# Optimization experiments

Measured on AMD Instinct MI355X. Metric: run time of the kernel, lower is better.

Reference implementation:

```python
import jax, jax.numpy as jnp
import numpy as np

EPS = 1e-8
SCALE_FACTOR = 5.0
ITERS = 3

def _ln(x, g, b):
    m = x.mean(-1, keepdims=True)
    v = ((x - m) ** 2).mean(-1, keepdims=True)
    return (x - m) / jnp.sqrt(v + 1e-5) * g + b

def setup_inputs() -> dict:
    key = jax.random.key(0)
    ks = jax.random.split(key, 12)
    B, N, K, D = 8, 1024, 8, 256
    n01 = lambda k, s, sc=0.02: jax.random.normal(k, s, jnp.float32) * sc
    return {
        "inputs": jax.random.normal(ks[0], (B, N, D), jnp.float32),
        "conditioning": jax.random.normal(ks[1], (B, K, D + 4), jnp.float32),
        "ni_g": jnp.ones((D,), jnp.float32), "ni_b": jnp.zeros((D,), jnp.float32),
        "ns_g": jnp.ones((D,), jnp.float32), "ns_b": jnp.zeros((D,), jnp.float32),
        "wq": n01(ks[2], (D, D)), "wk": n01(ks[3], (D, D)), "wv": n01(ks[4], (D, D)),
        "gp_w": n01(ks[5], (2, D), 0.5), "gp_b": jnp.zeros((D,), jnp.float32),
        "ge_ln_g": jnp.ones((D,), jnp.float32), "ge_ln_b": jnp.zeros((D,), jnp.float32),
        "ge_w1": n01(ks[6], (D, 2 * D)), "ge_b1": jnp.zeros((2 * D,), jnp.float32),
        "ge_w2": n01(ks[7], (2 * D, D)), "ge_b2": jnp.zeros((D,), jnp.float32),
        "gru_wih": n01(ks[8], (3 * D, D)), "gru_whh": n01(ks[9], (3 * D, D)),
        "gru_bih": jnp.zeros((3 * D,), jnp.float32), "gru_bhh": jnp.zeros((3 * D,), jnp.float32),
    }

def _forward(inputs, conditioning, ni_g, ni_b, ns_g, ns_b, wq, wk, wv,
             gp_w, gp_b, ge_ln_g, ge_ln_b, ge_w1, ge_b1, ge_w2, ge_b2,
             gru_wih, gru_whh, gru_bih, gru_bhh):
    B, N, FD = inputs.shape
    D = wq.shape[1]
    attn_scale = D ** -0.5
    side = int(round(N ** 0.5))
    xs = jnp.linspace(-1.0, 1.0, side)
    abs_grid = jnp.stack(jnp.meshgrid(xs, xs, indexing="ij"), -1).reshape(N, 2)  # (N,2)

    x = _ln(inputs, ni_g, ni_b)
    k = x @ wk  # (B,N,D)
    v = x @ wv  # (B,N,D)

    def grid_enc(t):
        h = _ln(t, ge_ln_g, ge_ln_b)
        h = jax.nn.relu(h @ ge_w1 + ge_b1)
        return h @ ge_w2 + ge_b2

    def step(slots_full, update):
        slots = slots_full[..., :-4]                       # (B,K,D)
        pos = jnp.clip(slots_full[..., -4:-2], -1.0, 1.0)  # (B,K,2)
        scl = jnp.clip(slots_full[..., -2:], 1e-3, 2.0)    # (B,K,2)
        rel_grid = (abs_grid[None, None] - pos[:, :, None]) / (scl[:, :, None] * SCALE_FACTOR)  # (B,K,N,2)
        rel_enc = rel_grid @ gp_w + gp_b                   # (B,K,N,D)
        rel_k = grid_enc(k[:, None] + rel_enc)             # (B,K,N,D)
        rel_v = grid_enc(v[:, None] + rel_enc)             # (B,K,N,D)
        q = _ln(slots, ns_g, ns_b) @ wq                    # (B,K,D)
        dots = jnp.einsum("bkd,bknd->bkn", q, rel_k) * attn_scale
        attn0 = jax.nn.softmax(dots, axis=1)               # softmax over the SLOT axis
        attn = attn0 + EPS
        attn = attn / attn.sum(-1, keepdims=True)
        pos_n = jnp.einsum("bkn,nd->bkd", attn0, abs_grid)
        spread = (abs_grid[None, None] - pos_n[:, :, None]) ** 2  # (B,K,N,2)
        scl_n = jnp.clip(jnp.sqrt(jnp.einsum("bkn,bknd->bkd", attn0 + EPS, spread)), 1e-3, 2.0)
        if update:
            upd = jnp.einsum("bknd,bkn->bkd", rel_v, attn)
            gx = upd @ gru_wih.T + gru_bih
            gh = slots @ gru_whh.T + gru_bhh
            xr, xz, xn = jnp.split(gx, 3, -1)
            hr, hz, hn = jnp.split(gh, 3, -1)
            r = jax.nn.sigmoid(xr + hr)
            z = jax.nn.sigmoid(xz + hz)
            n_ = jnp.tanh(xn + r * hn)
            slots = (1.0 - z) * n_ + z * slots
        return jnp.concatenate([slots, pos_n, scl_n], -1), attn0, rel_grid

    attn0 = rel_grid = None
    for i in range(ITERS + 1):
        conditioning, attn0, rel_grid = step(conditioning, i < ITERS)
    return conditioning, attn0, rel_grid

def reference(inputs, conditioning, ni_g, ni_b, ns_g, ns_b, wq, wk, wv,
              gp_w, gp_b, ge_ln_g, ge_ln_b, ge_w1, ge_b1, ge_w2, ge_b2,
              gru_wih, gru_whh, gru_bih, gru_bhh):
    return _forward(inputs, conditioning, ni_g, ni_b, ns_g, ns_b, wq, wk, wv,
                    gp_w, gp_b, ge_ln_g, ge_ln_b, ge_w1, ge_b1, ge_w2, ge_b2,
                    gru_wih, gru_whh, gru_bih, gru_bhh)
```

## Files before the change

### kernel.cpp

```cpp
#include <hip/hip_runtime.h>
#include <math.h>

#define NB 8
#define NN 1024
#define NK 8
#define ND 256
#define ND2 512
#define NBK 64
#define EPSA 1e-8f
#define LNEPS 1e-5f
#define GSTEP (2.0f/31.0f)

using short8 = __attribute__((ext_vector_type(8))) short;
using short4v = __attribute__((ext_vector_type(4))) short;
using floatx4 = __attribute__((ext_vector_type(4))) float;

__device__ __forceinline__ short f2bf(float f) {
  unsigned u = __builtin_bit_cast(unsigned, f);
  u += 0x7fffu + ((u >> 16) & 1u);
  return (short)(u >> 16);
}
__device__ __forceinline__ float bf2f(short s) {
  unsigned u = ((unsigned)(unsigned short)s) << 16;
  return __builtin_bit_cast(float, u);
}

__global__ __launch_bounds__(256) void k_cvt_all(
    const float* __restrict__ w1, const float* __restrict__ w2,
    const float* __restrict__ wk, const float* __restrict__ wv,
    const float* __restrict__ wih, const float* __restrict__ whh,
    const float* __restrict__ wq, const float* __restrict__ b2,
    const float* __restrict__ gpw, const float* __restrict__ lng,
    const float* __restrict__ lnb, const float* __restrict__ b1,
    short* __restrict__ w1T, short* __restrict__ wkT, short* __restrict__ wvT,
    short* __restrict__ whhp, short* __restrict__ w2B,
    float* __restrict__ bx, float* __restrict__ vb, float* __restrict__ vecs) {
  __shared__ float redS[4][32];
  const int blk = blockIdx.x;
  const int t = threadIdx.x;
  if (blk < 576) {
    const int id4 = blk * 256 + t;
    if (id4 < 32768) {
      const int i = id4 * 4;
      const int k = i >> 9, n0 = i & 511;
      const float4 v = *(const float4*)(w1 + (size_t)k * 512 + n0);
      const float vv[4] = {v.x, v.y, v.z, v.w};
#pragma unroll
      for (int q = 0; q < 4; q++) {
        const int n = n0 + q;
        const int dst = ((n >> 4) * 8 + (k >> 5)) * 512 + ((k >> 3) & 3) * 128 + (n & 15) * 8 + (k & 7);
        w1T[dst] = f2bf(vv[q]);
      }
    } else if (id4 < 49152) {
      const int i = (id4 - 32768) * 4;
      const int k = i >> 8, n0 = i & 255;
      const float4 v = *(const float4*)(wk + (size_t)k * 256 + n0);
      const float vv[4] = {v.x, v.y, v.z, v.w};
#pragma unroll
      for (int q = 0; q < 4; q++) {
        const int n = n0 + q;
        const int dst = ((n >> 4) * 8 + (k >> 5)) * 512 + ((k >> 3) & 3) * 128 + (n & 15) * 8 + (k & 7);
        wkT[dst] = f2bf(vv[q]);
      }
    } else if (id4 < 65536) {
      const int i = (id4 - 49152) * 4;
      const int k = i >> 8, n0 = i & 255;
      const float4 v = *(const float4*)(wv + (size_t)k * 256 + n0);
      const float vv[4] = {v.x, v.y, v.z, v.w};
#pragma unroll
      for (int q = 0; q < 4; q++) {
        const int n = n0 + q;
        const int dst = ((n >> 4) * 8 + (k >> 5)) * 512 + ((k >> 3) & 3) * 128 + (n & 15) * 8 + (k & 7);
        wvT[dst] = f2bf(vv[q]);
      }
    } else if (id4 < 114688) {
      const int i = (id4 - 65536) * 4;
      const int j = i >> 8, d0 = i & 255;
      const float4 v = *(const float4*)(whh + i);
      short4v pk = {f2bf(v.x), f2bf(v.y), f2bf(v.z), f2bf(v.w)};
      *(short4v*)&whhp[(size_t)((d0 >> 3) * 768 + j) * 8 + (d0 & 7)] = pk;
    } else {
      const int i = (id4 - 114688) * 4;
      const float4 v = *(const float4*)(w2 + i);
      short4v pk = {f2bf(v.x), f2bf(v.y), f2bf(v.z), f2bf(v.w)};
      *(short4v*)&w2B[i] = pk;
    }
  } else {
    const int fb = blk - 576;
    if (fb < 24) {
      const int o = t >> 3, sub = t & 7;
      const int j = fb * 32 + o;
      float p = 0.f;
#pragma unroll
      for (int q = 0; q < 8; q++) {
        const int d = sub * 32 + q * 4;
        const float4 wv4 = *(const float4*)(wih + (size_t)j * 256 + d);
        const float4 b4 = *(const float4*)(b2 + d);
        p += wv4.x * b4.x + wv4.y * b4.y + wv4.z * b4.z + wv4.w * b4.w;
      }
      p += __shfl_xor(p, 1); p += __shfl_xor(p, 2); p += __shfl_xor(p, 4);
      if (sub == 0) bx[j] = p;
    } else if (fb < 32) {
      const int o = t >> 3, sub = t & 7;
      const int e = (fb - 24) * 32 + o;
      float p = 0.f;
#pragma unroll
      for (int q = 0; q < 8; q++) {
        const int d = sub * 32 + q * 4;
        const float4 wv4 = *(const float4*)(wq + (size_t)e * 256 + d);
        const float4 b4 = *(const float4*)(b2 + d);
        p += wv4.x * b4.x + wv4.y * b4.y + wv4.z * b4.z + wv4.w * b4.w;
      }
      p += __shfl_xor(p, 1); p += __shfl_xor(p, 2); p += __shfl_xor(p, 4);
      if (sub == 0) vb[e] = p;
    } else if (fb < 96) {
      const int v = (fb - 32) >> 4;
      const int j0 = ((fb - 32) & 15) * 32;
      const int sub = t >> 5, o = t & 31;
      const int j = j0 + o;
      float p = 0.f;
#pragma unroll 8
      for (int q = 0; q < 32; q++) {
        const int d = sub * 32 + q;
        float c;
        if (v == 0) c = gpw[d] * lng[d];
        else if (v == 1) c = gpw[256 + d] * lng[d];
        else if (v == 2) c = lng[d];
        else c = lnb[d];
        p = fmaf(c, w1[(size_t)d * 512 + j], p);
      }
      p += __shfl_xor(p, 32);
      const int w = t >> 6;
      if ((t & 32) == 0) redS[w][o] = p;
      __syncthreads();
      if (t < 32) {
        float s = redS[0][t] + redS[1][t] + redS[2][t] + redS[3][t];
        if (v == 3) s += b1[j0 + t];
        vecs[v * 512 + j0 + t] = s;
      }
    } else {
      const float wa = gpw[t], wb = gpw[256 + t];
      float v0 = wa, v1 = wb, v2 = wa * wa, v3 = wb * wb, v4 = wa * wb;
#pragma unroll
      for (int m = 32; m >= 1; m >>= 1) {
        v0 += __shfl_xor(v0, m); v1 += __shfl_xor(v1, m); v2 += __shfl_xor(v2, m);
        v3 += __shfl_xor(v3, m); v4 += __shfl_xor(v4, m);
      }
      const int wv2 = t >> 6;
      if ((t & 63) == 0) {
        redS[wv2][0] = v0; redS[wv2][1] = v1; redS[wv2][2] = v2;
        redS[wv2][3] = v3; redS[wv2][4] = v4;
      }
      __syncthreads();
      if (t < 5)
        vecs[2048 + t] = (redS[0][t] + redS[1][t] + redS[2][t] + redS[3][t]) * (1.0f / 256.0f);
    }
  }
}

__global__ __launch_bounds__(256, 2) void k_mm(
    const float* __restrict__ wih, const float* __restrict__ wq,
    const short* __restrict__ w2B,
    short* __restrict__ WXTp, short* __restrict__ MQp) {
  const int z = blockIdx.z;
  if (z == 1 && blockIdx.x >= 4) return;
  const float* __restrict__ A = z ? wq : wih;
  __shared__ __align__(16) short As[64 * 264];
  const int row0 = blockIdx.x * 64;
  const int col0 = blockIdx.y * 128;
  const int t = threadIdx.x;
  const int wave = t >> 6, lane = t & 63, l15 = lane & 15, quad = lane >> 4;
  {
    const int r = t >> 2, sub = t & 3;
    const float* ar = A + (size_t)(row0 + r) * 256;
#pragma unroll
    for (int ii = 0; ii < 16; ii++) {
      const int d = sub * 4 + ii * 16;
      const float4 v = *(const float4*)(ar + d);
      short4v pk = {f2bf(v.x), f2bf(v.y), f2bf(v.z), f2bf(v.w)};
      *(short4v*)&As[r * 264 + d] = pk;
    }
  }
  __syncthreads();
  const short* wp = w2B + (size_t)(col0 + wave * 32 + l15) * 256 + quad * 8;
  floatx4 acc[4][2];
#pragma unroll
  for (int mt = 0; mt < 4; mt++)
#pragma unroll
    for (int nt = 0; nt < 2; nt++) acc[mt][nt] = (floatx4){0.f, 0.f, 0.f, 0.f};
#pragma unroll
  for (int kk = 0; kk < 8; kk++) {
    short8 af[4];
#pragma unroll
    for (int mt = 0; mt < 4; mt++)
      af[mt] = *(const short8*)&As[(mt * 16 + l15) * 264 + kk * 32 + quad * 8];
    short8 bf[2];
#pragma unroll
    for (int nt = 0; nt < 2; nt++)
      bf[nt] = *(const short8*)(wp + nt * 16 * 256 + kk * 32);
#pragma unroll
    for (int mt = 0; mt < 4; mt++)
#pragma unroll
      for (int nt = 0; nt < 2; nt++)
        acc[mt][nt] = __builtin_amdgcn_mfma_f32_16x16x32_bf16(af[mt], bf[nt], acc[mt][nt], 0, 0, 0);
  }
#pragma unroll
  for (int mt = 0; mt < 4; mt++)
#pragma unroll
    for (int nt = 0; nt < 2; nt++)
#pragma unroll
      for (int j = 0; j < 4; j++) {
        const int row = row0 + mt * 16 + quad * 4 + j;
        const int col = col0 + wave * 32 + nt * 16 + l15;
        const short val = f2bf(acc[mt][nt][j]);
        if (z) MQp[(size_t)((row >> 3) * 512 + col) * 8 + (row & 7)] = val;
        else   WXTp[(size_t)((col >> 3) * 768 + row) * 8 + (col & 7)] = val;
      }
}

__global__ __launch_bounds__(256, 2) void k_kv_kw(
    const float* __restrict__ inp,
    const float* __restrict__ nig, const float* __restrict__ nib,
    const short* __restrict__ wkT, const short* __restrict__ wvT,
    const float* __restrict__ gpb, const float* __restrict__ gpw,
    const float* __restrict__ lng,
    const short* __restrict__ w1T,
    short* __restrict__ KWk, short* __restrict__ KWv,
    float* __restrict__ momk, float* __restrict__ momv) {
  __shared__ __align__(16) short tln[64 * 264];
  __shared__ float momS[64][4][4];
  const short* __restrict__ WT = blockIdx.z ? wvT : wkT;
  short* __restrict__ KW = blockIdx.z ? KWv : KWk;
  float* __restrict__ mom = blockIdx.z ? momv : momk;
  const int row0 = blockIdx.x * 64;
  const int t = threadIdx.x;
  const int wave = t >> 6, lane = t & 63, l15 = lane & 15, quad = lane >> 4;
  {
    const int r = t >> 2, sub = t & 3;
    const float* xr = inp + (size_t)(row0 + r) * ND;
    float tv[64];
    float sum = 0.f, ssq = 0.f;
#pragma unroll
    for (int ii = 0; ii < 16; ii++) {
      const int d = sub * 4 + ii * 16;
      const float4 xv = *(const float4*)(xr + d);
      tv[ii * 4 + 0] = xv.x; sum += xv.x; ssq += xv.x * xv.x;
      tv[ii * 4 + 1] = xv.y; sum += xv.y; ssq += xv.y * xv.y;
      tv[ii * 4 + 2] = xv.z; sum += xv.z; ssq += xv.z * xv.z;
      tv[ii * 4 + 3] = xv.w; sum += xv.w; ssq += xv.w * xv.w;
    }
    sum += __shfl_xor(sum, 1); ssq += __shfl_xor(ssq, 1);
    sum += __shfl_xor(sum, 2); ssq += __shfl_xor(ssq, 2);
    const float mean = sum * (1.0f / ND);
    const float var = ssq * (1.0f / ND) - mean * mean;
    const float rstd = rsqrtf(var + LNEPS);
#pragma unroll
    for (int ii = 0; ii < 16; ii++) {
      const int d = sub * 4 + ii * 16;
      const float4 gg = *(const float4*)(nig + d);
      const float4 bb = *(const float4*)(nib + d);
      short4v pk;
      pk.x = f2bf((tv[ii * 4 + 0] - mean) * rstd * gg.x + bb.x);
      pk.y = f2bf((tv[ii * 4 + 1] - mean) * rstd * gg.y + bb.y);
      pk.z = f2bf((tv[ii * 4 + 2] - mean) * rstd * gg.z + bb.z);
      pk.w = f2bf((tv[ii * 4 + 3] - mean) * rstd * gg.w + bb.w);
      *(short4v*)&tln[r * 264 + d] = pk;
    }
  }
  __syncthreads();
  floatx4 acc[4][4];
#pragma unroll
  for (int mt = 0; mt < 4; mt++)
#pragma unroll
    for (int nt = 0; nt < 4; nt++) acc[mt][nt] = (floatx4){0.f, 0.f, 0.f, 0.f};
  {
    const short* wp = WT + (size_t)(wave * 32) * 512 + (size_t)lane * 8;
#pragma unroll
    for (int kk = 0; kk < 8; kk++) {
      short8 af[4];
#pragma unroll
      for (int mt = 0; mt < 4; mt++)
        af[mt] = *(const short8*)&tln[(mt * 16 + l15) * 264 + kk * 32 + quad * 8];
      short8 bf[4];
#pragma unroll
      for (int nt = 0; nt < 4; nt++)
        bf[nt] = *(const short8*)(wp + (nt * 8 + kk) * 512);
#pragma unroll
      for (int mt = 0; mt < 4; mt++)
#pragma unroll
        for (int nt = 0; nt < 4; nt++)
          acc[mt][nt] = __builtin_amdgcn_mfma_f32_16x16x32_bf16(af[mt], bf[nt], acc[mt][nt], 0, 0, 0);
    }
  }
  __syncthreads();
  {
    float waL[4], wbL[4], ggL[4], pbL[4];
#pragma unroll
    for (int nt = 0; nt < 4; nt++) {
      const int c = wave * 64 + nt * 16 + l15;
      waL[nt] = gpw[c]; wbL[nt] = gpw[256 + c];
      ggL[nt] = lng[c]; pbL[nt] = gpb[c];
    }
#pragma unroll
    for (int mt = 0; mt < 4; mt++)
#pragma unroll
      for (int j = 0; j < 4; j++) {
        const int row = mt * 16 + quad * 4 + j;
        float su = 0.f, sq = 0.f, sa = 0.f, sb = 0.f;
#pragma unroll
        for (int nt = 0; nt < 4; nt++) {
          const float u = acc[mt][nt][j] + pbL[nt];
          su += u; sq += u * u; sa += u * waL[nt]; sb += u * wbL[nt];
          tln[row * 264 + wave * 64 + nt * 16 + l15] = f2bf(u * ggL[nt]);
        }
        su += __shfl_xor(su, 1); sq += __shfl_xor(sq, 1);
        sa += __shfl_xor(sa, 1); sb += __shfl_xor(sb, 1);
        su += __shfl_xor(su, 2); sq += __shfl_xor(sq, 2);
        sa += __shfl_xor(sa, 2); sb += __shfl_xor(sb, 2);
        su += __shfl_xor(su, 4); sq += __shfl_xor(sq, 4);
        sa += __shfl_xor(sa, 4); sb += __shfl_xor(sb, 4);
        su += __shfl_xor(su, 8); sq += __shfl_xor(sq, 8);
        sa += __shfl_xor(sa, 8); sb += __shfl_xor(sb, 8);
        if (l15 == 0) {
          momS[row][wave][0] = su; momS[row][wave][1] = sq;
          momS[row][wave][2] = sa; momS[row][wave][3] = sb;
        }
      }
  }
  __syncthreads();
  if (t < 64) {
    const float m0 = momS[t][0][0] + momS[t][1][0] + momS[t][2][0] + momS[t][3][0];
    const float m1 = momS[t][0][1] + momS[t][1][1] + momS[t][2][1] + momS[t][3][1];
    const float m2 = momS[t][0][2] + momS[t][1][2] + momS[t][2][2] + momS[t][3][2];
    const float m3 = momS[t][0][3] + momS[t][1][3] + momS[t][2][3] + momS[t][3][3];
    float* mp = mom + (size_t)(row0 + t) * 4;
    mp[0] = m0 * (1.0f / ND); mp[1] = m1 * (1.0f / ND);
    mp[2] = m2 * (1.0f / ND); mp[3] = m3 * (1.0f / ND);
  }
  floatx4 acc2[4][8];
#pragma unroll
  for (int mt = 0; mt < 4; mt++)
#pragma unroll
    for (int nt = 0; nt < 8; nt++) acc2[mt][nt] = (floatx4){0.f, 0.f, 0.f, 0.f};
  const short* w1p = w1T + (size_t)(wave * 64) * 512 + (size_t)lane * 8;
#pragma unroll
  for (int kk = 0; kk < 8; kk++) {
    short8 af[4];
#pragma unroll
    for (int mt = 0; mt < 4; mt++)
      af[mt] = *(const short8*)&tln[(mt * 16 + l15) * 264 + kk * 32 + quad * 8];
    short8 bf[8];
#pragma unroll
    for (int nt = 0; nt < 8; nt++)
      bf[nt] = *(const short8*)(w1p + (nt * 8 + kk) * 512);
#pragma unroll
    for (int mt = 0; mt < 4; mt++)
#pragma unroll
      for (int nt = 0; nt < 8; nt++)
        acc2[mt][nt] = __builtin_amdgcn_mfma_f32_16x16x32_bf16(af[mt], bf[nt], acc2[mt][nt], 0, 0, 0);
  }
#pragma unroll
  for (int mt = 0; mt < 4; mt++)
#pragma unroll
    for (int nt = 0; nt < 8; nt++)
#pragma unroll
      for (int j = 0; j < 4; j++)
        KW[(size_t)(row0 + mt * 16 + quad * 4 + j) * 512 + wave * 128 + nt * 16 + l15] =
            f2bf(acc2[mt][nt][j]);
}

__global__ __launch_bounds__(256) void k_dots(
    const short* __restrict__ KW, const float* __restrict__ mom,
    const float* __restrict__ vecs,
    const float* __restrict__ pos, const float* __restrict__ scl,
    const float* __restrict__ w2q, const float* __restrict__ stage,
    float* __restrict__ dots) {
  const int b = blockIdx.y, nt = blockIdx.x, kk0 = blockIdx.z * 4;
  const int t = threadIdx.x, wave = t >> 6, lane = t & 63;
  float AWv[8], BWv[8], GWv[8], bWv[8];
#pragma unroll
  for (int e = 0; e < 8; e++) {
    const int j = e * 64 + lane;
    AWv[e] = vecs[j]; BWv[e] = vecs[512 + j];
    GWv[e] = vecs[1024 + j]; bWv[e] = vecs[1536 + j];
  }
  const float mwa = vecs[2048], mwb = vecs[2049];
  const float ewa2 = vecs[2050], ewb2 = vecs[2051], ewab = vecs[2052];
  float p0[4], p1[4], si0[4], si1[4], qb2[4];
#pragma unroll
  for (int k = 0; k < 4; k++) {
    const int bk = b * 8 + kk0 + k;
    p0[k] = pos[bk * 2]; p1[k] = pos[bk * 2 + 1];
    si0[k] = 1.0f / (scl[bk * 2] * 5.0f);
    si1[k] = 1.0f / (scl[bk * 2 + 1] * 5.0f);
    qb2[k] = stage[bk * 8 + 5];
  }
#pragma unroll
  for (int i = 0; i < 2; i++) {
    const int n = nt * 8 + wave * 2 + i;
    const int row = b * NN + n;
    float KWr[8];
#pragma unroll
    for (int e = 0; e < 8; e++) KWr[e] = bf2f(KW[(size_t)row * 512 + e * 64 + lane]);
    const float mu = mom[row * 4 + 0], qm = mom[row * 4 + 1];
    const float ca = mom[row * 4 + 2], cb = mom[row * 4 + 3];
    const float gx = -1.0f + GSTEP * (float)(n >> 5);
    const float gy = -1.0f + GSTEP * (float)(n & 31);
#pragma unroll
    for (int k = 0; k < 4; k++) {
      const float rg0 = (gx - p0[k]) * si0[k];
      const float rg1 = (gy - p1[k]) * si1[k];
      const float mean = mu + rg0 * mwa + rg1 * mwb;
      const float ey2 = qm + rg0 * rg0 * ewa2 + rg1 * rg1 * ewb2 +
                        2.0f * (rg0 * ca + rg1 * cb + rg0 * rg1 * ewab);
      const float rstd = rsqrtf(ey2 - mean * mean + LNEPS);
      const float* wq = w2q + (size_t)(b * 8 + kk0 + k) * 512;
      float d = 0.f;
#pragma unroll
      for (int e = 0; e < 8; e++) {
        float tt = KWr[e];
        tt = fmaf(rg0, AWv[e], tt);
        tt = fmaf(rg1, BWv[e], tt);
        tt = fmaf(-mean, GWv[e], tt);
        const float h = fmaf(rstd, tt, bWv[e]);
        d = fmaf(fmaxf(h, 0.f), wq[e * 64 + lane], d);
      }
      d += __shfl_xor(d, 1); d += __shfl_xor(d, 2); d += __shfl_xor(d, 4);
      d += __shfl_xor(d, 8); d += __shfl_xor(d, 16); d += __shfl_xor(d, 32);
      if (lane == 0) dots[(size_t)(b * 8 + kk0 + k) * NN + n] = (d + qb2[k]) * 0.0625f;
    }
  }
}

__global__ __launch_bounds__(256) void k_ph(
    const short* __restrict__ KW, const float* __restrict__ mom,
    const float* __restrict__ vecs,
    const float* __restrict__ pos, const float* __restrict__ scl,
    const float* __restrict__ attn0, float* __restrict__ php) {
  const int b = blockIdx.y, nt = blockIdx.x, kk0 = blockIdx.z * 4;
  const int t = threadIdx.x, wave = t >> 6, lane = t & 63;
  __shared__ float phs[4 * 512];
  float AWv[8], BWv[8], GWv[8], bWv[8];
#pragma unroll
  for (int e = 0; e < 8; e++) {
    const int j = e * 64 + lane;
    AWv[e] = vecs[j]; BWv[e] = vecs[512 + j];
    GWv[e] = vecs[1024 + j]; bWv[e] = vecs[1536 + j];
  }
  const float mwa = vecs[2048], mwb = vecs[2049];
  const float ewa2 = vecs[2050], ewb2 = vecs[2051], ewab = vecs[2052];
  float p0[4], p1[4], si0[4], si1[4];
#pragma unroll
  for (int k = 0; k < 4; k++) {
    const int bk = b * 8 + kk0 + k;
    p0[k] = pos[bk * 2]; p1[k] = pos[bk * 2 + 1];
    si0[k] = 1.0f / (scl[bk * 2] * 5.0f);
    si1[k] = 1.0f / (scl[bk * 2 + 1] * 5.0f);
  }
  float acc[4][8];
#pragma unroll
  for (int k = 0; k < 4; k++)
#pragma unroll
    for (int e = 0; e < 8; e++) acc[k][e] = 0.f;
#pragma unroll
  for (int i = 0; i < 4; i++) {
    const int n = nt * 16 + wave * 4 + i;
    const int row = b * NN + n;
    float KWr[8];
#pragma unroll
    for (int e = 0; e < 8; e++) KWr[e] = bf2f(KW[(size_t)row * 512 + e * 64 + lane]);
    const float mu = mom[row * 4 + 0], qm = mom[row * 4 + 1];
    const float ca = mom[row * 4 + 2], cb = mom[row * 4 + 3];
    const float gx = -1.0f + GSTEP * (float)(n >> 5);
    const float gy = -1.0f + GSTEP * (float)(n & 31);
#pragma unroll
    for (int k = 0; k < 4; k++) {
      const float rg0 = (gx - p0[k]) * si0[k];
      const float rg1 = (gy - p1[k]) * si1[k];
      const float mean = mu + rg0 * mwa + rg1 * mwb;
      const float ey2 = qm + rg0 * rg0 * ewa2 + rg1 * rg1 * ewb2 +
                        2.0f * (rg0 * ca + rg1 * cb + rg0 * rg1 * ewab);
      const float rstd = rsqrtf(ey2 - mean * mean + LNEPS);
      const float aw = attn0[(size_t)(b * 8 + kk0 + k) * NN + n] + EPSA;
#pragma unroll
      for (int e = 0; e < 8; e++) {
        float tt = KWr[e];
        tt = fmaf(rg0, AWv[e], tt);
        tt = fmaf(rg1, BWv[e], tt);
        tt = fmaf(-mean, GWv[e], tt);
        const float h = fmaf(rstd, tt, bWv[e]);
        acc[k][e] = fmaf(aw, fmaxf(h, 0.f), acc[k][e]);
      }
    }
  }
#pragma unroll
  for (int w = 0; w < 4; w++) {
    if (wave == w) {
#pragma unroll
      for (int k = 0; k < 4; k++)
#pragma unroll
        for (int e = 0; e < 8; e++) {
          const int j = e * 64 + lane;
          if (w == 0) phs[k * 512 + j] = acc[k][e];
          else phs[k * 512 + j] += acc[k][e];
        }
    }
    __syncthreads();
  }
  float* dst = php + (size_t)(((nt * 8 + b) * 8) + kk0) * 512;
  const int base = t * 8;
  *(float4*)(dst + base) = *(const float4*)(phs + base);
  *(float4*)(dst + base + 4) = *(const float4*)(phs + base + 4);
}

__global__ __launch_bounds__(64) void k_softmax_reduce(
    const float* __restrict__ dots, float* __restrict__ attn0,
    float* __restrict__ stage) {
  const int t = threadIdx.x;
  const int idx = blockIdx.x * 64 + t;
  const int b = idx >> 10, n = idx & 1023;
  float vals[NK];
  float mx = -1e30f;
#pragma unroll
  for (int k = 0; k < NK; k++) {
    vals[k] = dots[(size_t)(b * NK + k) * NN + n];
    mx = fmaxf(mx, vals[k]);
  }
  float s = 0.f;
#pragma unroll
  for (int k = 0; k < NK; k++) { vals[k] = expf(vals[k] - mx); s += vals[k]; }
  const float inv = 1.0f / s;
  const float gx = -1.0f + GSTEP * (float)(n >> 5);
  const float gy = -1.0f + GSTEP * (float)(n & 31);
  const float gx2 = gx * gx, gy2 = gy * gy;
  float sk[NK][5];
#pragma unroll
  for (int k = 0; k < NK; k++) {
    const float a = vals[k] * inv;
    attn0[(size_t)(b * NK + k) * NN + n] = a;
    const float w = a + EPSA;
    sk[k][0] = a;
    sk[k][1] = a * gx;
    sk[k][2] = a * gy;
    sk[k][3] = w * gx2;
    sk[k][4] = w * gy2;
  }
#pragma unroll
  for (int m = 32; m >= 1; m >>= 1)
#pragma unroll
    for (int k = 0; k < NK; k++)
#pragma unroll
      for (int c = 0; c < 5; c++)
        sk[k][c] += __shfl_xor(sk[k][c], m);
  __shared__ float red[40];
  if (t == 0) {
#pragma unroll
    for (int k = 0; k < NK; k++)
#pragma unroll
      for (int c = 0; c < 5; c++)
        red[k * 5 + c] = sk[k][c];
  }
  __syncthreads();
  if (t < 40) {
    const int k = t / 5, c = t % 5;
    atomicAdd(&stage[(b * NK + k) * 8 + c], red[t]);
  }
}

__global__ __launch_bounds__(256) void k_tail(
    const float* __restrict__ php, float* __restrict__ sf,
    const short* __restrict__ WXTp, const short* __restrict__ whhp,
    const float* __restrict__ bx,
    const float* __restrict__ bih, const float* __restrict__ bhh,
    const float* __restrict__ nsg, const float* __restrict__ nsb,
    const short* __restrict__ MQp, const float* __restrict__ vb,
    float* __restrict__ w2q, float* __restrict__ pos, float* __restrict__ scl,
    float* __restrict__ stage) {
  const int bk = blockIdx.x, t = threadIdx.x;
  const int b = bk >> 3, k = bk & 7;
  __shared__ float phv[512];
  __shared__ float sfv[256];
  __shared__ float lnvS[256];
  __shared__ float red[8];
  const int wv = t >> 6;
  sfv[t] = sf[bk * 260 + t];
  const float dn = 1.0f / (stage[bk * 8 + 0] + (float)NN * EPSA);
  float s0 = 0.f, s1 = 0.f;
#pragma unroll 4
  for (int p = 0; p < 64; p++) {
    const float* src = php + (size_t)((p * 8 + b) * 8 + k) * 512;
    s0 += src[t];
    s1 += src[t + 256];
  }
  phv[t] = s0 * dn;
  phv[t + 256] = s1 * dn;
  __syncthreads();
  float x0 = bx[t], x1 = bx[256 + t], x2 = bx[512 + t];
#pragma unroll 4
  for (int e8 = 0; e8 < 64; e8++) {
    const float4 pa = *(const float4*)&phv[e8 * 8];
    const float4 pb4 = *(const float4*)&phv[e8 * 8 + 4];
    const float pv[8] = {pa.x, pa.y, pa.z, pa.w, pb4.x, pb4.y, pb4.z, pb4.w};
    const short8 wr0 = *(const short8*)&WXTp[(size_t)(e8 * 768 + t) * 8];
    const short8 wr1 = *(const short8*)&WXTp[(size_t)(e8 * 768 + 256 + t) * 8];
    const short8 wr2 = *(const short8*)&WXTp[(size_t)(e8 * 768 + 512 + t) * 8];
#pragma unroll
    for (int r = 0; r < 8; r++) {
      x0 = fmaf(pv[r], bf2f(wr0[r]), x0);
      x1 = fmaf(pv[r], bf2f(wr1[r]), x1);
      x2 = fmaf(pv[r], bf2f(wr2[r]), x2);
    }
  }
  float h0 = 0.f, h1v = 0.f, h2 = 0.f;
#pragma unroll 4
  for (int d8 = 0; d8 < 32; d8++) {
    const float4 sa = *(const float4*)&sfv[d8 * 8];
    const float4 sb4 = *(const float4*)&sfv[d8 * 8 + 4];
    const float sv[8] = {sa.x, sa.y, sa.z, sa.w, sb4.x, sb4.y, sb4.z, sb4.w};
    const short8 hr0 = *(const short8*)&whhp[(size_t)(d8 * 768 + t) * 8];
    const short8 hr1 = *(const short8*)&whhp[(size_t)(d8 * 768 + 256 + t) * 8];
    const short8 hr2 = *(const short8*)&whhp[(size_t)(d8 * 768 + 512 + t) * 8];
#pragma unroll
    for (int r = 0; r < 8; r++) {
      h0 = fmaf(sv[r], bf2f(hr0[r]), h0);
      h1v = fmaf(sv[r], bf2f(hr1[r]), h1v);
      h2 = fmaf(sv[r], bf2f(hr2[r]), h2);
    }
  }
  const float r = 1.0f / (1.0f + expf(-(x0 + bih[t] + h0 + bhh[t])));
  const float z = 1.0f / (1.0f + expf(-(x1 + bih[256 + t] + h1v + bhh[256 + t])));
  const float nw = tanhf(x2 + bih[512 + t] + r * (h2 + bhh[512 + t]));
  const float ns = (1.0f - z) * nw + z * sfv[t];
  sf[bk * 260 + t] = ns;
  float s2 = ns, ss = ns * ns;
#pragma unroll
  for (int m = 32; m >= 1; m >>= 1) { s2 += __shfl_xor(s2, m); ss += __shfl_xor(ss, m); }
  if ((t & 63) == 0) { red[wv] = s2; red[4 + wv] = ss; }
  __syncthreads();
  const float S = red[0] + red[1] + red[2] + red[3];
  const float SS = red[4] + red[5] + red[6] + red[7];
  const float mean = S * (1.0f / ND);
  const float var = SS * (1.0f / ND) - mean * mean;
  const float rstd = rsqrtf(var + LNEPS);
  const float lnv = (ns - mean) * rstd * nsg[t] + nsb[t];
  lnvS[t] = lnv;
  if (t == 0) {
    const float Sa = stage[bk * 8 + 0];
    const float G0 = stage[bk * 8 + 1];
    const float G1 = stage[bk * 8 + 2];
    const float Q0 = stage[bk * 8 + 3];
    const float Q1 = stage[bk * 8 + 4];
    const float W = Sa + (float)NN * EPSA;
    const float sc0 = sqrtf(fmaxf(Q0 - 2.0f * G0 * G0 + G0 * G0 * W, 0.f));
    const float sc1 = sqrtf(fmaxf(Q1 - 2.0f * G1 * G1 + G1 * G1 * W, 0.f));
    const float sc0c = fminf(fmaxf(sc0, 1e-3f), 2.0f);
    const float sc1c = fminf(fmaxf(sc1, 1e-3f), 2.0f);
    sf[bk * 260 + 256] = G0;
    sf[bk * 260 + 257] = G1;
    sf[bk * 260 + 258] = sc0c;
    sf[bk * 260 + 259] = sc1c;
    pos[bk * 2 + 0] = fminf(fmaxf(G0, -1.0f), 1.0f);
    pos[bk * 2 + 1] = fminf(fmaxf(G1, -1.0f), 1.0f);
    scl[bk * 2 + 0] = sc0c;
    scl[bk * 2 + 1] = sc1c;
  }
  __syncthreads();
  if (t < 5) stage[bk * 8 + t] = 0.f;
  float w0 = 0.f, w1v = 0.f;
#pragma unroll 4
  for (int e8 = 0; e8 < 32; e8++) {
    const float4 la = *(const float4*)&lnvS[e8 * 8];
    const float4 lb = *(const float4*)&lnvS[e8 * 8 + 4];
    const float lv[8] = {la.x, la.y, la.z, la.w, lb.x, lb.y, lb.z, lb.w};
    const short8 m0 = *(const short8*)&MQp[(size_t)(e8 * 512 + t) * 8];
    const short8 m1 = *(const short8*)&MQp[(size_t)(e8 * 512 + 256 + t) * 8];
#pragma unroll
    for (int rr = 0; rr < 8; rr++) {
      w0 = fmaf(lv[rr], bf2f(m0[rr]), w0);
      w1v = fmaf(lv[rr], bf2f(m1[rr]), w1v);
    }
  }
  w2q[bk * 512 + t] = w0;
  w2q[bk * 512 + 256 + t] = w1v;
  float qd = lnvS[t] * vb[t];
#pragma unroll
  for (int m = 32; m >= 1; m >>= 1) qd += __shfl_xor(qd, m);
  __syncthreads();
  if ((t & 63) == 0) red[wv] = qd;
  __syncthreads();
  if (t == 0) stage[bk * 8 + 5] = red[0] + red[1] + red[2] + red[3];
}

__global__ __launch_bounds__(256) void k_slot0(
    float* __restrict__ sf, const float* __restrict__ cond,
    const float* __restrict__ nsg, const float* __restrict__ nsb,
    const short* __restrict__ MQp, const float* __restrict__ vb,
    float* __restrict__ w2q, float* __restrict__ pos, float* __restrict__ scl,
    float* __restrict__ stage) {
  const int bk = blockIdx.x, t = threadIdx.x;
  __shared__ float lnvS[256];
  __shared__ float red[8];
  const int wv = t >> 6;
  const float ns = cond[bk * 260 + t];
  sf[bk * 260 + t] = ns;
  if (t < 4) sf[bk * 260 + 256 + t] = cond[bk * 260 + 256 + t];
  float s2 = ns, ss = ns * ns;
#pragma unroll
  for (int m = 32; m >= 1; m >>= 1) { s2 += __shfl_xor(s2, m); ss += __shfl_xor(ss, m); }
  if ((t & 63) == 0) { red[wv] = s2; red[4 + wv] = ss; }
  __syncthreads();
  const float S = red[0] + red[1] + red[2] + red[3];
  const float SS = red[4] + red[5] + red[6] + red[7];
  const float mean = S * (1.0f / ND);
  const float var = SS * (1.0f / ND) - mean * mean;
  const float rstd = rsqrtf(var + LNEPS);
  const float lnv = (ns - mean) * rstd * nsg[t] + nsb[t];
  lnvS[t] = lnv;
  if (t < 2) {
    const float p = cond[bk * 260 + 256 + t];
    pos[bk * 2 + t] = fminf(fmaxf(p, -1.0f), 1.0f);
    const float sc = cond[bk * 260 + 258 + t];
    scl[bk * 2 + t] = fminf(fmaxf(sc, 1e-3f), 2.0f);
  }
  __syncthreads();
  if (t < 5) stage[bk * 8 + t] = 0.f;
  float w0 = 0.f, w1v = 0.f;
#pragma unroll 4
  for (int e8 = 0; e8 < 32; e8++) {
    const float4 la = *(const float4*)&lnvS[e8 * 8];
    const float4 lb = *(const float4*)&lnvS[e8 * 8 + 4];
    const float lv[8] = {la.x, la.y, la.z, la.w, lb.x, lb.y, lb.z, lb.w};
    const short8 m0 = *(const short8*)&MQp[(size_t)(e8 * 512 + t) * 8];
    const short8 m1 = *(const short8*)&MQp[(size_t)(e8 * 512 + 256 + t) * 8];
#pragma unroll
    for (int rr = 0; rr < 8; rr++) {
      w0 = fmaf(lv[rr], bf2f(m0[rr]), w0);
      w1v = fmaf(lv[rr], bf2f(m1[rr]), w1v);
    }
  }
  w2q[bk * 512 + t] = w0;
  w2q[bk * 512 + 256 + t] = w1v;
  float qd = lnvS[t] * vb[t];
#pragma unroll
  for (int m = 32; m >= 1; m >>= 1) qd += __shfl_xor(qd, m);
  __syncthreads();
  if ((t & 63) == 0) red[wv] = qd;
  __syncthreads();
  if (t == 0) stage[bk * 8 + 5] = red[0] + red[1] + red[2] + red[3];
}

__global__ __launch_bounds__(256) void k_finalize(
    const float* __restrict__ sf, const float* __restrict__ attn0,
    const float* __restrict__ pos, const float* __restrict__ scl,
    const float* __restrict__ stage, float* __restrict__ out) {
  const int bk = blockIdx.x, t = threadIdx.x;
  out[bk * 260 + t] = sf[bk * 260 + t];
  if (t == 0) {
    const float Sa = stage[bk * 8 + 0];
    const float G0 = stage[bk * 8 + 1];
    const float G1 = stage[bk * 8 + 2];
    const float Q0 = stage[bk * 8 + 3];
    const float Q1 = stage[bk * 8 + 4];
    const float W = Sa + (float)NN * EPSA;
    const float sc0 = sqrtf(fmaxf(Q0 - 2.0f * G0 * G0 + G0 * G0 * W, 0.f));
    const float sc1 = sqrtf(fmaxf(Q1 - 2.0f * G1 * G1 + G1 * G1 * W, 0.f));
    out[bk * 260 + 256] = G0;
    out[bk * 260 + 257] = G1;
    out[bk * 260 + 258] = fminf(fmaxf(sc0, 1e-3f), 2.0f);
    out[bk * 260 + 259] = fminf(fmaxf(sc1, 1e-3f), 2.0f);
  }
  const float p0 = pos[bk * 2 + 0], p1 = pos[bk * 2 + 1];
  const float s0 = scl[bk * 2 + 0] * 5.0f, s1 = scl[bk * 2 + 1] * 5.0f;
#pragma unroll
  for (int i = 0; i < 4; i++) {
    const int n = t + 256 * i;
    out[16640 + bk * NN + n] = attn0[(size_t)bk * NN + n];
    const float gx = -1.0f + GSTEP * (float)(n >> 5);
    const float gy = -1.0f + GSTEP * (float)(n & 31);
    float2 v;
    v.x = (gx - p0) / s0;
    v.y = (gy - p1) / s1;
    *(float2*)(out + 16640 + 65536 + ((size_t)bk * NN + n) * 2) = v;
  }
}

extern "C" void kernel_launch(void* const* d_in, const int* in_sizes, int n_in,
                              void* d_out, int out_size, void* d_ws, size_t ws_size,
                              hipStream_t stream) {
  const float* inputs   = (const float*)d_in[0];
  const float* cond     = (const float*)d_in[1];
  const float* ni_g     = (const float*)d_in[2];
  const float* ni_b     = (const float*)d_in[3];
  const float* ns_g     = (const float*)d_in[4];
  const float* ns_b     = (const float*)d_in[5];
  const float* wq       = (const float*)d_in[6];
  const float* wk       = (const float*)d_in[7];
  const float* wv       = (const float*)d_in[8];
  const float* gp_w     = (const float*)d_in[9];
  const float* gp_b     = (const float*)d_in[10];
  const float* ge_ln_g  = (const float*)d_in[11];
  const float* ge_ln_b  = (const float*)d_in[12];
  const float* ge_w1    = (const float*)d_in[13];
  const float* ge_b1    = (const float*)d_in[14];
  const float* ge_w2    = (const float*)d_in[15];
  const float* ge_b2    = (const float*)d_in[16];
  const float* gru_wih  = (const float*)d_in[17];
  const float* gru_whh  = (const float*)d_in[18];
  const float* gru_bih  = (const float*)d_in[19];
  const float* gru_bhh  = (const float*)d_in[20];

  float* ws   = (float*)d_ws;
  float* php  = ws;
  float* sf   = php + 2097152;
  float* w2qb = sf + 16640;
  float* posb = w2qb + 32768;
  float* sclb = posb + 128;
  float* dotsb = sclb + 128;
  float* at0  = dotsb + 65536;
  float* stag = at0 + 65536;
  float* bxb  = stag + 512;
  float* vbb  = bxb + 768;
  float* momk = vbb + 256;
  float* momv = momk + 32768;
  float* vecs = momv + 32768;
  short* w1T  = (short*)(vecs + 2560);
  short* wkT  = w1T + 131072;
  short* wvT  = wkT + 65536;
  short* whhp = wvT + 65536;
  short* w2B  = whhp + 196608;
  short* WXTp = w2B + 131072;
  short* MQp  = WXTp + 393216;
  short* KWk  = MQp + 131072;
  short* KWv  = KWk + 4194304;

  float* out = (float*)d_out;

  k_cvt_all<<<673, 256, 0, stream>>>(ge_w1, ge_w2, wk, wv, gru_wih, gru_whh, wq,
                                     ge_b2, gp_w, ge_ln_g, ge_ln_b, ge_b1,
                                     w1T, wkT, wvT, whhp, w2B, bxb, vbb, vecs);
  k_mm<<<dim3(12, 4, 2), 256, 0, stream>>>(gru_wih, wq, w2B, WXTp, MQp);
  k_kv_kw<<<dim3(128, 1, 2), 256, 0, stream>>>(inputs, ni_g, ni_b, wkT, wvT,
                                               gp_b, gp_w, ge_ln_g, w1T,
                                               KWk, KWv, momk, momv);
  k_slot0<<<NBK, 256, 0, stream>>>(sf, cond, ns_g, ns_b, MQp, vbb,
                                   w2qb, posb, sclb, stag);

  for (int s = 0; s < 4; s++) {
    k_dots<<<dim3(128, NB, 2), 256, 0, stream>>>(KWk, momk, vecs, posb, sclb,
                                                 w2qb, stag, dotsb);
    k_softmax_reduce<<<128, 64, 0, stream>>>(dotsb, at0, stag);
    if (s < 3) {
      k_ph<<<dim3(64, NB, 2), 256, 0, stream>>>(KWv, momv, vecs, posb, sclb,
                                                at0, php);
      k_tail<<<NBK, 256, 0, stream>>>(php, sf, WXTp, whhp, bxb,
                                      gru_bih, gru_bhh, ns_g, ns_b, MQp, vbb,
                                      w2qb, posb, sclb, stag);
    }
  }

  k_finalize<<<NBK, 256, 0, stream>>>(sf, at0, posb, sclb, stag, out);
}
```

Before: 371.5 us.

## Fuse dots, softmax and weighted-sum kernels into one per-iteration kernel

Adds a k_iter kernel that, for each grid row, computes the attention logits for all 8 slots, applies the softmax in registers and immediately accumulates the attention-weighted value features. It also accumulates the per-slot attention moments into the stage buffer with atomicAdd. This removes the separate dots, softmax and ph launches, along with the global round trip of logits and attention, inside the three update iterations. The cost is twice as many partial-sum slices for k_tail to reduce, heavier per-block register use, and reliance on the stage moment slots being zeroed before the atomics.

```diff
diff --git a/kernel.cpp b/kernel.cpp
--- a/kernel.cpp
+++ b/kernel.cpp
@@ -369,6 +369,153 @@
             f2bf(acc2[mt][nt][j]);
 }
 
+__global__ __launch_bounds__(256) void k_iter(
+    const short* __restrict__ KWk, const short* __restrict__ KWv,
+    const float* __restrict__ momk, const float* __restrict__ momv,
+    const float* __restrict__ vecs,
+    const float* __restrict__ pos, const float* __restrict__ scl,
+    const float* __restrict__ w2q, float* __restrict__ stage,
+    float* __restrict__ php) {
+  const int b = blockIdx.y, nt = blockIdx.x;
+  const int t = threadIdx.x, wave = t >> 6, lane = t & 63;
+  __shared__ float w2qS[8 * 512];
+  __shared__ float momRed[4][40];
+#pragma unroll
+  for (int q = 0; q < 16; q++)
+    w2qS[q * 256 + t] = w2q[(size_t)b * 4096 + q * 256 + t];
+  __syncthreads();
+  float AWv[8], BWv[8], GWv[8], bWv[8];
+#pragma unroll
+  for (int e = 0; e < 8; e++) {
+    const int j = e * 64 + lane;
+    AWv[e] = vecs[j]; BWv[e] = vecs[512 + j];
+    GWv[e] = vecs[1024 + j]; bWv[e] = vecs[1536 + j];
+  }
+  const float mwa = vecs[2048], mwb = vecs[2049];
+  const float ewa2 = vecs[2050], ewb2 = vecs[2051], ewab = vecs[2052];
+  float p0[8], p1[8], si0[8], si1[8], qb2[8];
+#pragma unroll
+  for (int k = 0; k < 8; k++) {
+    const int bk = b * 8 + k;
+    p0[k] = pos[bk * 2]; p1[k] = pos[bk * 2 + 1];
+    si0[k] = 1.0f / (scl[bk * 2] * 5.0f);
+    si1[k] = 1.0f / (scl[bk * 2 + 1] * 5.0f);
+    qb2[k] = stage[bk * 8 + 5];
+  }
+  float acc[8][8];
+#pragma unroll
+  for (int k = 0; k < 8; k++)
+#pragma unroll
+    for (int e = 0; e < 8; e++) acc[k][e] = 0.f;
+  float msum = 0.f;
+  const int mk = lane / 5, mc = lane - mk * 5;
+#pragma unroll
+  for (int i = 0; i < 2; i++) {
+    const int n = nt * 8 + wave * 2 + i;
+    const int row = b * NN + n;
+    const float gx = -1.0f + GSTEP * (float)(n >> 5);
+    const float gy = -1.0f + GSTEP * (float)(n & 31);
+    float KWr[8];
+#pragma unroll
+    for (int e = 0; e < 8; e++) KWr[e] = bf2f(KWk[(size_t)row * 512 + e * 64 + lane]);
+    {
+      const float mu = momk[row * 4 + 0], qm = momk[row * 4 + 1];
+      const float ca = momk[row * 4 + 2], cb = momk[row * 4 + 3];
+      float dk[8];
+#pragma unroll
+      for (int k = 0; k < 8; k++) {
+        const float rg0 = (gx - p0[k]) * si0[k];
+        const float rg1 = (gy - p1[k]) * si1[k];
+        const float mean = mu + rg0 * mwa + rg1 * mwb;
+        const float ey2 = qm + rg0 * rg0 * ewa2 + rg1 * rg1 * ewb2 +
+                          2.0f * (rg0 * ca + rg1 * cb + rg0 * rg1 * ewab);
+        const float rstd = rsqrtf(ey2 - mean * mean + LNEPS);
+        float d = 0.f;
+#pragma unroll
+        for (int e = 0; e < 8; e++) {
+          float tt = KWr[e];
+          tt = fmaf(rg0, AWv[e], tt);
+          tt = fmaf(rg1, BWv[e], tt);
+          tt = fmaf(-mean, GWv[e], tt);
+          const float h = fmaf(rstd, tt, bWv[e]);
+          d = fmaf(fmaxf(h, 0.f), w2qS[k * 512 + e * 64 + lane], d);
+        }
+        d += __shfl_xor(d, 1); d += __shfl_xor(d, 2); d += __shfl_xor(d, 4);
+        d += __shfl_xor(d, 8); d += __shfl_xor(d, 16); d += __shfl_xor(d, 32);
+        dk[k] = (d + qb2[k]) * 0.0625f;
+      }
+      float mx = dk[0];
+#pragma unroll
+      for (int k = 1; k < 8; k++) mx = fmaxf(mx, dk[k]);
+      float s = 0.f;
+#pragma unroll
+      for (int k = 0; k < 8; k++) { dk[k] = expf(dk[k] - mx); s += dk[k]; }
+      const float inv = 1.0f / s;
+#pragma unroll
+      for (int k = 0; k < 8; k++) dk[k] *= inv;
+      if (lane < 40) {
+        const float a = dk[mk];
+        float mval;
+        if (mc == 0) mval = a;
+        else if (mc == 1) mval = a * gx;
+        else if (mc == 2) mval = a * gy;
+        else if (mc == 3) mval = (a + EPSA) * gx * gx;
+        else mval = (a + EPSA) * gy * gy;
+        msum += mval;
+      }
+#pragma unroll
+      for (int e = 0; e < 8; e++) KWr[e] = bf2f(KWv[(size_t)row * 512 + e * 64 + lane]);
+      const float mu2 = momv[row * 4 + 0], qm2 = momv[row * 4 + 1];
+      const float ca2 = momv[row * 4 + 2], cb2 = momv[row * 4 + 3];
+#pragma unroll
+      for (int k = 0; k < 8; k++) {
+        const float rg0 = (gx - p0[k]) * si0[k];
+        const float rg1 = (gy - p1[k]) * si1[k];
+        const float mean = mu2 + rg0 * mwa + rg1 * mwb;
+        const float ey2 = qm2 + rg0 * rg0 * ewa2 + rg1 * rg1 * ewb2 +
+                          2.0f * (rg0 * ca2 + rg1 * cb2 + rg0 * rg1 * ewab);
+        const float rstd = rsqrtf(ey2 - mean * mean + LNEPS);
+        const float aw = dk[k] + EPSA;
+#pragma unroll
+        for (int e = 0; e < 8; e++) {
+          float tt = KWr[e];
+          tt = fmaf(rg0, AWv[e], tt);
+          tt = fmaf(rg1, BWv[e], tt);
+          tt = fmaf(-mean, GWv[e], tt);
+          const float h = fmaf(rstd, tt, bWv[e]);
+          acc[k][e] = fmaf(aw, fmaxf(h, 0.f), acc[k][e]);
+        }
+      }
+    }
+  }
+  if (lane < 40) momRed[wave][lane] = msum;
+  __syncthreads();
+  if (t < 40) {
+    const float tot = momRed[0][t] + momRed[1][t] + momRed[2][t] + momRed[3][t];
+    atomicAdd(&stage[(b * 8 + t / 5) * 8 + (t % 5)], tot);
+  }
+  float* phs = w2qS;
+#pragma unroll
+  for (int w = 0; w < 4; w++) {
+    if (wave == w) {
+#pragma unroll
+      for (int k = 0; k < 8; k++)
+#pragma unroll
+        for (int e = 0; e < 8; e++) {
+          const int j = k * 512 + e * 64 + lane;
+          if (w == 0) phs[j] = acc[k][e];
+          else phs[j] += acc[k][e];
+        }
+    }
+    __syncthreads();
+  }
+  float* dst = php + (size_t)((nt * 8 + b) * 8) * 512;
+  const int base = t * 16;
+#pragma unroll
+  for (int q = 0; q < 4; q++)
+    *(float4*)(dst + base + q * 4) = *(const float4*)(phs + base + q * 4);
+}
+
 __global__ __launch_bounds__(256) void k_dots(
     const short* __restrict__ KW, const float* __restrict__ mom,
     const float* __restrict__ vecs,
@@ -430,87 +577,6 @@
       if (lane == 0) dots[(size_t)(b * 8 + kk0 + k) * NN + n] = (d + qb2[k]) * 0.0625f;
     }
   }
-}
-
-__global__ __launch_bounds__(256) void k_ph(
-    const short* __restrict__ KW, const float* __restrict__ mom,
-    const float* __restrict__ vecs,
-    const float* __restrict__ pos, const float* __restrict__ scl,
-    const float* __restrict__ attn0, float* __restrict__ php) {
-  const int b = blockIdx.y, nt = blockIdx.x, kk0 = blockIdx.z * 4;
-  const int t = threadIdx.x, wave = t >> 6, lane = t & 63;
-  __shared__ float phs[4 * 512];
-  float AWv[8], BWv[8], GWv[8], bWv[8];
-#pragma unroll
-  for (int e = 0; e < 8; e++) {
-    const int j = e * 64 + lane;
-    AWv[e] = vecs[j]; BWv[e] = vecs[512 + j];
-    GWv[e] = vecs[1024 + j]; bWv[e] = vecs[1536 + j];
-  }
-  const float mwa = vecs[2048], mwb = vecs[2049];
-  const float ewa2 = vecs[2050], ewb2 = vecs[2051], ewab = vecs[2052];
-  float p0[4], p1[4], si0[4], si1[4];
-#pragma unroll
-  for (int k = 0; k < 4; k++) {
-    const int bk = b * 8 + kk0 + k;
-    p0[k] = pos[bk * 2]; p1[k] = pos[bk * 2 + 1];
-    si0[k] = 1.0f / (scl[bk * 2] * 5.0f);
-    si1[k] = 1.0f / (scl[bk * 2 + 1] * 5.0f);
-  }
-  float acc[4][8];
-#pragma unroll
-  for (int k = 0; k < 4; k++)
-#pragma unroll
-    for (int e = 0; e < 8; e++) acc[k][e] = 0.f;
-#pragma unroll
-  for (int i = 0; i < 4; i++) {
-    const int n = nt * 16 + wave * 4 + i;
-    const int row = b * NN + n;
-    float KWr[8];
-#pragma unroll
-    for (int e = 0; e < 8; e++) KWr[e] = bf2f(KW[(size_t)row * 512 + e * 64 + lane]);
-    const float mu = mom[row * 4 + 0], qm = mom[row * 4 + 1];
-    const float ca = mom[row * 4 + 2], cb = mom[row * 4 + 3];
-    const float gx = -1.0f + GSTEP * (float)(n >> 5);
-    const float gy = -1.0f + GSTEP * (float)(n & 31);
-#pragma unroll
-    for (int k = 0; k < 4; k++) {
-      const float rg0 = (gx - p0[k]) * si0[k];
-      const float rg1 = (gy - p1[k]) * si1[k];
-      const float mean = mu + rg0 * mwa + rg1 * mwb;
-      const float ey2 = qm + rg0 * rg0 * ewa2 + rg1 * rg1 * ewb2 +
-                        2.0f * (rg0 * ca + rg1 * cb + rg0 * rg1 * ewab);
-      const float rstd = rsqrtf(ey2 - mean * mean + LNEPS);
-      const float aw = attn0[(size_t)(b * 8 + kk0 + k) * NN + n] + EPSA;
-#pragma unroll
-      for (int e = 0; e < 8; e++) {
-        float tt = KWr[e];
-        tt = fmaf(rg0, AWv[e], tt);
-        tt = fmaf(rg1, BWv[e], tt);
-        tt = fmaf(-mean, GWv[e], tt);
-        const float h = fmaf(rstd, tt, bWv[e]);
-        acc[k][e] = fmaf(aw, fmaxf(h, 0.f), acc[k][e]);
-      }
-    }
-  }
-#pragma unroll
-  for (int w = 0; w < 4; w++) {
-    if (wave == w) {
-#pragma unroll
-      for (int k = 0; k < 4; k++)
-#pragma unroll
-        for (int e = 0; e < 8; e++) {
-          const int j = e * 64 + lane;
-          if (w == 0) phs[k * 512 + j] = acc[k][e];
-          else phs[k * 512 + j] += acc[k][e];
-        }
-    }
-    __syncthreads();
-  }
-  float* dst = php + (size_t)(((nt * 8 + b) * 8) + kk0) * 512;
-  const int base = t * 8;
-  *(float4*)(dst + base) = *(const float4*)(phs + base);
-  *(float4*)(dst + base + 4) = *(const float4*)(phs + base + 4);
 }
 
 __global__ __launch_bounds__(64) void k_softmax_reduce(
@@ -587,7 +653,7 @@
   const float dn = 1.0f / (stage[bk * 8 + 0] + (float)NN * EPSA);
   float s0 = 0.f, s1 = 0.f;
 #pragma unroll 4
-  for (int p = 0; p < 64; p++) {
+  for (int p = 0; p < 128; p++) {
     const float* src = php + (size_t)((p * 8 + b) * 8 + k) * 512;
     s0 += src[t];
     s1 += src[t + 256];
@@ -811,7 +877,7 @@
 
   float* ws   = (float*)d_ws;
   float* php  = ws;
-  float* sf   = php + 2097152;
+  float* sf   = php + 4194304;
   float* w2qb = sf + 16640;
   float* posb = w2qb + 32768;
   float* sclb = posb + 128;
@@ -845,18 +911,16 @@
   k_slot0<<<NBK, 256, 0, stream>>>(sf, cond, ns_g, ns_b, MQp, vbb,
                                    w2qb, posb, sclb, stag);
 
-  for (int s = 0; s < 4; s++) {
-    k_dots<<<dim3(128, NB, 2), 256, 0, stream>>>(KWk, momk, vecs, posb, sclb,
-                                                 w2qb, stag, dotsb);
-    k_softmax_reduce<<<128, 64, 0, stream>>>(dotsb, at0, stag);
-    if (s < 3) {
-      k_ph<<<dim3(64, NB, 2), 256, 0, stream>>>(KWv, momv, vecs, posb, sclb,
-                                                at0, php);
-      k_tail<<<NBK, 256, 0, stream>>>(php, sf, WXTp, whhp, bxb,
-                                      gru_bih, gru_bhh, ns_g, ns_b, MQp, vbb,
-                                      w2qb, posb, sclb, stag);
-    }
-  }
+  for (int s = 0; s < 3; s++) {
+    k_iter<<<dim3(128, NB), 256, 0, stream>>>(KWk, KWv, momk, momv, vecs,
+                                              posb, sclb, w2qb, stag, php);
+    k_tail<<<NBK, 256, 0, stream>>>(php, sf, WXTp, whhp, bxb,
+                                    gru_bih, gru_bhh, ns_g, ns_b, MQp, vbb,
+                                    w2qb, posb, sclb, stag);
+  }
+  k_dots<<<dim3(128, NB, 2), 256, 0, stream>>>(KWk, momk, vecs, posb, sclb,
+                                               w2qb, stag, dotsb);
+  k_softmax_reduce<<<128, 64, 0, stream>>>(dotsb, at0, stag);
 
   k_finalize<<<NBK, 256, 0, stream>>>(sf, at0, posb, sclb, stag, out);
 }
```

New measurement: 393.0 us. 5.8% more time.

## Fuse slot-attention dot products with softmax and moment reduction

Applied to the files above, without the earlier changes.

Merges the dots kernel and the separate softmax/moment-reduction kernel into one kernel in which each block handles all 8 slots for its 8 positions. The softmax and the per-slot moment sums are computed in registers, then reduced per wave and per block through shared memory before the atomic adds. The w2q weights for the batch are staged in shared memory first. This removes one launch per iteration and the round trip of the dots buffer through global memory, at the cost of halving the grid and raising per-thread work and register use. It also raises the unroll factor of the k_tail accumulation loop.

```diff
diff --git a/kernel.cpp b/kernel.cpp
--- a/kernel.cpp
+++ b/kernel.cpp
@@ -369,14 +369,20 @@
             f2bf(acc2[mt][nt][j]);
 }
 
-__global__ __launch_bounds__(256) void k_dots(
-    const short* __restrict__ KW, const float* __restrict__ mom,
+__global__ __launch_bounds__(256) void k_dotsm(
+    const short* __restrict__ KWk, const float* __restrict__ momk,
     const float* __restrict__ vecs,
     const float* __restrict__ pos, const float* __restrict__ scl,
-    const float* __restrict__ w2q, const float* __restrict__ stage,
-    float* __restrict__ dots) {
-  const int b = blockIdx.y, nt = blockIdx.x, kk0 = blockIdx.z * 4;
+    const float* __restrict__ w2q, float* __restrict__ stage,
+    float* __restrict__ attn0) {
+  const int b = blockIdx.y, nt = blockIdx.x;
   const int t = threadIdx.x, wave = t >> 6, lane = t & 63;
+  __shared__ float w2qS[8 * 512];
+  __shared__ float momRed[4][40];
+#pragma unroll
+  for (int q = 0; q < 16; q++)
+    w2qS[q * 256 + t] = w2q[(size_t)b * 4096 + q * 256 + t];
+  __syncthreads();
   float AWv[8], BWv[8], GWv[8], bWv[8];
 #pragma unroll
   for (int e = 0; e < 8; e++) {
@@ -386,35 +392,37 @@
   }
   const float mwa = vecs[2048], mwb = vecs[2049];
   const float ewa2 = vecs[2050], ewb2 = vecs[2051], ewab = vecs[2052];
-  float p0[4], p1[4], si0[4], si1[4], qb2[4];
-#pragma unroll
-  for (int k = 0; k < 4; k++) {
-    const int bk = b * 8 + kk0 + k;
+  float p0[8], p1[8], si0[8], si1[8], qb2[8];
+#pragma unroll
+  for (int k = 0; k < 8; k++) {
+    const int bk = b * 8 + k;
     p0[k] = pos[bk * 2]; p1[k] = pos[bk * 2 + 1];
     si0[k] = 1.0f / (scl[bk * 2] * 5.0f);
     si1[k] = 1.0f / (scl[bk * 2 + 1] * 5.0f);
     qb2[k] = stage[bk * 8 + 5];
   }
+  float msum = 0.f;
+  const int mk = lane / 5, mc = lane - mk * 5;
 #pragma unroll
   for (int i = 0; i < 2; i++) {
     const int n = nt * 8 + wave * 2 + i;
     const int row = b * NN + n;
-    float KWr[8];
-#pragma unroll
-    for (int e = 0; e < 8; e++) KWr[e] = bf2f(KW[(size_t)row * 512 + e * 64 + lane]);
-    const float mu = mom[row * 4 + 0], qm = mom[row * 4 + 1];
-    const float ca = mom[row * 4 + 2], cb = mom[row * 4 + 3];
     const float gx = -1.0f + GSTEP * (float)(n >> 5);
     const float gy = -1.0f + GSTEP * (float)(n & 31);
-#pragma unroll
-    for (int k = 0; k < 4; k++) {
+    float KWr[8];
+#pragma unroll
+    for (int e = 0; e < 8; e++) KWr[e] = bf2f(KWk[(size_t)row * 512 + e * 64 + lane]);
+    const float mu = momk[row * 4 + 0], qm = momk[row * 4 + 1];
+    const float ca = momk[row * 4 + 2], cb = momk[row * 4 + 3];
+    float dk[8];
+#pragma unroll
+    for (int k = 0; k < 8; k++) {
       const float rg0 = (gx - p0[k]) * si0[k];
       const float rg1 = (gy - p1[k]) * si1[k];
       const float mean = mu + rg0 * mwa + rg1 * mwb;
       const float ey2 = qm + rg0 * rg0 * ewa2 + rg1 * rg1 * ewb2 +
                         2.0f * (rg0 * ca + rg1 * cb + rg0 * rg1 * ewab);
       const float rstd = rsqrtf(ey2 - mean * mean + LNEPS);
-      const float* wq = w2q + (size_t)(b * 8 + kk0 + k) * 512;
       float d = 0.f;
 #pragma unroll
       for (int e = 0; e < 8; e++) {
@@ -423,12 +431,40 @@
         tt = fmaf(rg1, BWv[e], tt);
         tt = fmaf(-mean, GWv[e], tt);
         const float h = fmaf(rstd, tt, bWv[e]);
-        d = fmaf(fmaxf(h, 0.f), wq[e * 64 + lane], d);
+        d = fmaf(fmaxf(h, 0.f), w2qS[k * 512 + e * 64 + lane], d);
       }
       d += __shfl_xor(d, 1); d += __shfl_xor(d, 2); d += __shfl_xor(d, 4);
       d += __shfl_xor(d, 8); d += __shfl_xor(d, 16); d += __shfl_xor(d, 32);
-      if (lane == 0) dots[(size_t)(b * 8 + kk0 + k) * NN + n] = (d + qb2[k]) * 0.0625f;
-    }
+      dk[k] = (d + qb2[k]) * 0.0625f;
+    }
+    float mx = dk[0];
+#pragma unroll
+    for (int k = 1; k < 8; k++) mx = fmaxf(mx, dk[k]);
+    float s = 0.f;
+#pragma unroll
+    for (int k = 0; k < 8; k++) { dk[k] = expf(dk[k] - mx); s += dk[k]; }
+    const float inv = 1.0f / s;
+#pragma unroll
+    for (int k = 0; k < 8; k++) {
+      dk[k] *= inv;
+      if (lane == 0) attn0[(size_t)(b * 8 + k) * NN + n] = dk[k];
+    }
+    if (lane < 40) {
+      const float a = dk[mk];
+      float mval;
+      if (mc == 0) mval = a;
+      else if (mc == 1) mval = a * gx;
+      else if (mc == 2) mval = a * gy;
+      else if (mc == 3) mval = (a + EPSA) * gx * gx;
+      else mval = (a + EPSA) * gy * gy;
+      msum += mval;
+    }
+  }
+  if (lane < 40) momRed[wave][lane] = msum;
+  __syncthreads();
+  if (t < 40) {
+    const float tot = momRed[0][t] + momRed[1][t] + momRed[2][t] + momRed[3][t];
+    atomicAdd(&stage[(b * 8 + t / 5) * 8 + (t % 5)], tot);
   }
 }
 
@@ -511,60 +547,6 @@
   const int base = t * 8;
   *(float4*)(dst + base) = *(const float4*)(phs + base);
   *(float4*)(dst + base + 4) = *(const float4*)(phs + base + 4);
-}
-
-__global__ __launch_bounds__(64) void k_softmax_reduce(
-    const float* __restrict__ dots, float* __restrict__ attn0,
-    float* __restrict__ stage) {
-  const int t = threadIdx.x;
-  const int idx = blockIdx.x * 64 + t;
-  const int b = idx >> 10, n = idx & 1023;
-  float vals[NK];
-  float mx = -1e30f;
-#pragma unroll
-  for (int k = 0; k < NK; k++) {
-    vals[k] = dots[(size_t)(b * NK + k) * NN + n];
-    mx = fmaxf(mx, vals[k]);
-  }
-  float s = 0.f;
-#pragma unroll
-  for (int k = 0; k < NK; k++) { vals[k] = expf(vals[k] - mx); s += vals[k]; }
-  const float inv = 1.0f / s;
-  const float gx = -1.0f + GSTEP * (float)(n >> 5);
-  const float gy = -1.0f + GSTEP * (float)(n & 31);
-  const float gx2 = gx * gx, gy2 = gy * gy;
-  float sk[NK][5];
-#pragma unroll
-  for (int k = 0; k < NK; k++) {
-    const float a = vals[k] * inv;
-    attn0[(size_t)(b * NK + k) * NN + n] = a;
-    const float w = a + EPSA;
-    sk[k][0] = a;
-    sk[k][1] = a * gx;
-    sk[k][2] = a * gy;
-    sk[k][3] = w * gx2;
-    sk[k][4] = w * gy2;
-  }
-#pragma unroll
-  for (int m = 32; m >= 1; m >>= 1)
-#pragma unroll
-    for (int k = 0; k < NK; k++)
-#pragma unroll
-      for (int c = 0; c < 5; c++)
-        sk[k][c] += __shfl_xor(sk[k][c], m);
-  __shared__ float red[40];
-  if (t == 0) {
-#pragma unroll
-    for (int k = 0; k < NK; k++)
-#pragma unroll
-      for (int c = 0; c < 5; c++)
-        red[k * 5 + c] = sk[k][c];
-  }
-  __syncthreads();
-  if (t < 40) {
-    const int k = t / 5, c = t % 5;
-    atomicAdd(&stage[(b * NK + k) * 8 + c], red[t]);
-  }
 }
 
 __global__ __launch_bounds__(256) void k_tail(
@@ -586,7 +568,7 @@
   sfv[t] = sf[bk * 260 + t];
   const float dn = 1.0f / (stage[bk * 8 + 0] + (float)NN * EPSA);
   float s0 = 0.f, s1 = 0.f;
-#pragma unroll 4
+#pragma unroll 8
   for (int p = 0; p < 64; p++) {
     const float* src = php + (size_t)((p * 8 + b) * 8 + k) * 512;
     s0 += src[t];
@@ -846,9 +828,8 @@
                                    w2qb, posb, sclb, stag);
 
   for (int s = 0; s < 4; s++) {
-    k_dots<<<dim3(128, NB, 2), 256, 0, stream>>>(KWk, momk, vecs, posb, sclb,
-                                                 w2qb, stag, dotsb);
-    k_softmax_reduce<<<128, 64, 0, stream>>>(dotsb, at0, stag);
+    k_dotsm<<<dim3(128, NB), 256, 0, stream>>>(KWk, momk, vecs, posb, sclb,
+                                               w2qb, stag, at0);
     if (s < 3) {
       k_ph<<<dim3(64, NB, 2), 256, 0, stream>>>(KWv, momv, vecs, posb, sclb,
                                                 at0, php);
```

After: 368.3 us (median of 2 runs). No clear change (-0.9%).
